# Optimization experiments

Hardware: AMD Instinct MI355X
Metric: run time of the kernel (lower is better)

Reference implementation:

```python
import jax, jax.numpy as jnp
import numpy as np

B, N, H = 8, 1024, 768
NUM_HEADS = 12
HEAD_DIM = H // NUM_HEADS
EDGE_VOCAB = 32
SCALE = 1.0 / np.sqrt(HEAD_DIM)


def setup_inputs() -> dict:
    key = jax.random.key(0)
    ks = jax.random.split(key, 12)
    s = 0.02
    return {
        "x": jax.random.normal(ks[0], (B, N, H), dtype=jnp.float32),
        "E": jax.random.randint(ks[1], (B, N, N), 0, EDGE_VOCAB, dtype=jnp.int64),
        "M": jax.random.randint(ks[2], (B, N), 0, 2, dtype=jnp.int32),
        "Wq": jax.random.normal(ks[3], (H, H), dtype=jnp.float32) * s,
        "bq": jnp.zeros((H,), dtype=jnp.float32),
        "Wk": jax.random.normal(ks[4], (H, H), dtype=jnp.float32) * s,
        "bk": jnp.zeros((H,), dtype=jnp.float32),
        "Wv": jax.random.normal(ks[5], (H, H), dtype=jnp.float32) * s,
        "bv": jnp.zeros((H,), dtype=jnp.float32),
        "Wo": jax.random.normal(ks[6], (H, H), dtype=jnp.float32) * s,
        "bo": jnp.zeros((H,), dtype=jnp.float32),
        "edge_emb": jax.random.normal(ks[7], (EDGE_VOCAB, NUM_HEADS), dtype=jnp.float32) * s,
    }


def reference(x, E, M, Wq, bq, Wk, bk, Wv, bv, Wo, bo, edge_emb):
    b, n, h = x.shape
    nh, hd = NUM_HEADS, HEAD_DIM
    # projections (y = x @ W + b, W stored as (in, out))
    Q = (x @ Wq + bq).reshape(b, n, nh, hd).transpose(0, 2, 1, 3)  # (B,h,N,d)
    K = (x @ Wk + bk).reshape(b, n, nh, hd).transpose(0, 2, 1, 3)
    V = (x @ Wv + bv).reshape(b, n, nh, hd).transpose(0, 2, 1, 3)
    scores = jnp.einsum('bhnd,bhmd->bhnm', Q, K) * SCALE
    # edge bias: (B,N,N) tokens -> (B,N,N,h) -> (B,h,N,N)
    bias = edge_emb[E].transpose(0, 3, 1, 2)
    scores = scores + bias
    # dual masking: mask key positions (M[j]==0) and query positions (M[i]==0)
    valid = (M[:, None, None, :] != 0) & (M[:, None, :, None] != 0)  # (B,1,N,N)
    scores = jnp.where(valid, scores, -1e9)
    attn = jax.nn.softmax(scores, axis=-1)
    out = jnp.einsum('bhnm,bhmd->bhnd', attn, V)
    out = out.transpose(0, 2, 1, 3).reshape(b, n, h)
    return out @ Wo + bo
```

## Files before the change

kernel.cpp:

```cpp
#include <hip/hip_runtime.h>
#include <stdint.h>

#define DEV __device__ __forceinline__

typedef __attribute__((ext_vector_type(8))) short bf16x8;
typedef __attribute__((ext_vector_type(4))) float f32x4;
typedef __attribute__((ext_vector_type(16))) float f32x16;

DEV unsigned short f2bf(float f) {
  union { float f; uint32_t u; } v; v.f = f;
  uint32_t r = v.u + 0x7fffu + ((v.u >> 16) & 1u);
  return (unsigned short)(r >> 16);
}

DEV void lds_load16(void* dst, const void* src) {
  __builtin_amdgcn_global_load_lds(
      (const __attribute__((address_space(1))) unsigned int*)src,
      (__attribute__((address_space(3))) unsigned int*)dst, 16, 0, 0);
}


__global__ void conv_x_k(const float* __restrict__ x, unsigned short* __restrict__ o) {
  const int i = blockIdx.x * 256 + threadIdx.x;
  const float4 v = ((const float4*)x)[i];
  ushort4 u;
  u.x = f2bf(v.x); u.y = f2bf(v.y); u.z = f2bf(v.z); u.w = f2bf(v.w);
  ((ushort4*)o)[i] = u;
}

__global__ void conv_E_k(const int* __restrict__ E, const int* __restrict__ Mm,
                         uint8_t* __restrict__ E8L) {
  const int tid = blockIdx.x * 256 + threadIdx.x;
  const int k4 = tid & 255;
  const int q = (tid >> 8) & 1023;
  const int b = tid >> 18;
  const uint4 e = ((const uint4*)E)[tid];
  const int mq = Mm[b * 1024 + q];
  const int4 mk = *(const int4*)&Mm[b * 1024 + k4 * 4];
  uint32_t r;
  {
    const uint32_t b0 = (mq && mk.x) ? (e.x & 31u) : 32u;
    const uint32_t b1 = (mq && mk.y) ? (e.y & 31u) : 32u;
    const uint32_t b2 = (mq && mk.z) ? (e.z & 31u) : 32u;
    const uint32_t b3 = (mq && mk.w) ? (e.w & 31u) : 32u;
    r = b0 | (b1 << 8) | (b2 << 16) | (b3 << 24);
  }
  const int kt = k4 >> 4;
  const int k4t = k4 & 15;
  const int h = k4t & 1, c = (k4t >> 1) & 3, a = k4t >> 3;
  const int lane = (h << 5) | (q & 31);
  const int qw = q >> 5;
  const int j = a * 4 + c;
  const size_t rec = ((((size_t)b * 32 + qw) * 16 + kt) * 64 + lane) * 32 + j * 4;
  *(uint32_t*)(E8L + rec) = r;
}

__global__ void transp_w_k(const float* __restrict__ Wq, const float* __restrict__ Wk,
                           const float* __restrict__ Wv, const float* __restrict__ Wo,
                           unsigned short* __restrict__ wtqkv, unsigned short* __restrict__ wot) {
  __shared__ float tile[64][65];
  const int z = blockIdx.z;
  const float* W = (z == 0) ? Wq : (z == 1) ? Wk : (z == 2) ? Wv : Wo;
  unsigned short* D = (z < 3) ? wtqkv + (size_t)z * 768 * 768 : wot;
  const int k0 = blockIdx.x * 64;
  const int c0 = blockIdx.y * 64;
  const int t = threadIdx.x;
#pragma unroll
  for (int i = 0; i < 4; ++i) {
    const int idx = i * 256 + t;
    const int r = idx >> 4;
    const int cq = (idx & 15) * 4;
    const float4 v = *(const float4*)&W[(k0 + r) * 768 + c0 + cq];
    tile[r][cq] = v.x; tile[r][cq + 1] = v.y; tile[r][cq + 2] = v.z; tile[r][cq + 3] = v.w;
  }
  __syncthreads();
#pragma unroll
  for (int i = 0; i < 4; ++i) {
    const int idx = i * 256 + t;
    const int c = idx >> 4;
    const int kq = (idx & 15) * 4;
    ushort4 u;
    u.x = f2bf(tile[kq][c]);     u.y = f2bf(tile[kq + 1][c]);
    u.z = f2bf(tile[kq + 2][c]); u.w = f2bf(tile[kq + 3][c]);
    *(ushort4*)&D[(c0 + c) * 768 + k0 + kq] = u;
  }
}

template <int MODE>
__global__ __launch_bounds__(256, 2)
void gemm_bt(const unsigned short* __restrict__ A, const unsigned short* __restrict__ Bt,
             const float* __restrict__ b0, const float* __restrict__ b1, const float* __restrict__ b2,
             unsigned short* __restrict__ Qb, unsigned short* __restrict__ Kb,
             unsigned short* __restrict__ Vt, float* __restrict__ Fo) {
  __shared__ __attribute__((aligned(16))) unsigned short lds[2][8192];
  const int t = threadIdx.x;
  const int lane = t & 63;
  const int wid = t >> 6;
  const int m0 = blockIdx.x * 128;
  const int n0 = blockIdx.y * 128;
  const int wm = (wid >> 1) * 64;
  const int wn = (wid & 1) * 64;
  const int srow = t & 127;
  const int sk8 = (t >> 7) * 8;

  const unsigned short* gA = A + (m0 + srow) * 768 + sk8;
  const unsigned short* gB = Bt + (n0 + srow) * 768 + sk8;

  const f32x4 Z4 = {0.f, 0.f, 0.f, 0.f};
  f32x4 acc[4][4];
#pragma unroll
  for (int m = 0; m < 4; ++m)
#pragma unroll
    for (int n = 0; n < 4; ++n) acc[m][n] = Z4;

  const int a_off = (lane >> 4) * 1024 + (wm + (lane & 15)) * 8;
  const int b_off = 4096 + (lane >> 4) * 1024 + (wn + (lane & 15)) * 8;

  auto stage = [&](int buf, int kt) {
    unsigned short* dA = &lds[buf][0] + wid * 512;
    unsigned short* dB = &lds[buf][4096] + wid * 512;
    const unsigned short* sA = gA + kt * 32;
    const unsigned short* sB = gB + kt * 32;
    lds_load16(dA, sA);
    lds_load16(dA + 2048, sA + 16);
    lds_load16(dB, sB);
    lds_load16(dB + 2048, sB + 16);
  };

  stage(0, 0);
  int cur = 0;
  for (int kt = 0; kt < 24; ++kt) {
    __syncthreads();
    if (kt + 1 < 24) stage(cur ^ 1, kt + 1);
    bf16x8 av[4], bvv[4];
#pragma unroll
    for (int m = 0; m < 4; ++m) av[m] = *(const bf16x8*)&lds[cur][a_off + m * 128];
#pragma unroll
    for (int n = 0; n < 4; ++n) bvv[n] = *(const bf16x8*)&lds[cur][b_off + n * 128];
#pragma unroll
    for (int m = 0; m < 4; ++m)
#pragma unroll
      for (int n = 0; n < 4; ++n)
        acc[m][n] = __builtin_amdgcn_mfma_f32_16x16x32_bf16(av[m], bvv[n], acc[m][n], 0, 0, 0);
    cur ^= 1;
  }

  const int g = lane >> 4;
  const int c15 = lane & 15;
  if (MODE == 1) {
#pragma unroll
    for (int n = 0; n < 4; ++n) {
      const int col = n0 + wn + n * 16 + c15;
      const float bval = b0[col];
#pragma unroll
      for (int m = 0; m < 4; ++m) {
        const int r0 = m0 + wm + m * 16 + g * 4;
#pragma unroll
        for (int r = 0; r < 4; ++r) Fo[(r0 + r) * 768 + col] = acc[m][n][r] + bval;
      }
    }
  } else {
    const int mat = blockIdx.y / 6;
    const float* bsel = (mat == 0) ? b0 : (mat == 1) ? b1 : b2;
    unsigned short* qk = (mat == 0) ? Qb : Kb;
#pragma unroll
    for (int n = 0; n < 4; ++n) {
      const int cw = (blockIdx.y % 6) * 128 + wn + n * 16 + c15;
      const int hh = cw >> 6, dd = cw & 63;
      const float bval = bsel[cw];
#pragma unroll
      for (int m = 0; m < 4; ++m) {
        const int r0 = m0 + wm + m * 16 + g * 4;
        const int bb = r0 >> 10;
        const int nn = r0 & 1023;
        if (mat < 2) {
          unsigned short* dst = qk + ((bb * 12 + hh) * 1024 + nn) * 64 + dd;
#pragma unroll
          for (int r = 0; r < 4; ++r) dst[r * 64] = f2bf(acc[m][n][r] + bval);
        } else {
          ushort4 w;
          w.x = f2bf(acc[m][n][0] + bval);
          w.y = f2bf(acc[m][n][1] + bval);
          w.z = f2bf(acc[m][n][2] + bval);
          w.w = f2bf(acc[m][n][3] + bval);
          *(ushort4*)&Vt[((bb * 12 + hh) * 64 + dd) * 1024 + nn] = w;
        }
      }
    }
  }
}

__global__ __launch_bounds__(256, 3)
void attn_fused(const unsigned short* __restrict__ Qb, const unsigned short* __restrict__ Kb,
                const unsigned short* __restrict__ Vt, const uint8_t* __restrict__ E8L,
                const float* __restrict__ emb, unsigned short* __restrict__ AO) {
  __shared__ __attribute__((aligned(16))) unsigned short Ks[2][4096];
  __shared__ __attribute__((aligned(16))) unsigned short Vs[2][4096];
  __shared__ float ttab[33];
  __shared__ float red[4][32];

  const int t = threadIdx.x;
  const int lane = t & 63;
  const int wid = t >> 6;
  const int l31 = lane & 31;
  const int hl = lane >> 5;

  const int id = blockIdx.x;
  const int sw = (id & 7) * 96 + (id >> 3);
  const int b = sw / 96;
  const int rem = sw - b * 96;
  const int h = rem >> 3;
  const int qb = rem & 7;
  const int bh = b * 12 + h;
  const int qw = qb * 4 + wid;
  const int q0 = qw * 32;

  if (t < 33) ttab[t] = (t < 32) ? emb[t * 12 + h] * 1.44269504f : -1e30f;

  bf16x8 qf[4];
  {
    const unsigned short* qp = Qb + ((size_t)bh * 1024 + q0 + l31) * 64 + hl * 8;
#pragma unroll
    for (int dc = 0; dc < 4; ++dc) qf[dc] = *(const bf16x8*)(qp + dc * 16);
  }

  auto stageKV = [&](int buf, int kt) {
#pragma unroll
    for (int i = 0; i < 2; ++i) {
      const int c = i * 256 + t;
      const int row = c >> 3, c16 = c & 7;
      const int sc = (c16 ^ (row & 7)) * 8;
      lds_load16(&Ks[buf][i * 2048 + wid * 512],
                 Kb + ((size_t)bh * 1024 + kt * 64 + row) * 64 + sc);
      lds_load16(&Vs[buf][i * 2048 + wid * 512],
                 Vt + ((size_t)bh * 64 + row) * 1024 + kt * 64 + sc);
    }
  };

  const uint8_t* ebase = E8L + (((size_t)(b * 32 + qw)) * 16 * 64 + lane) * 32;

  stageKV(0, 0);
  uint4 e0 = *(const uint4*)(ebase);
  uint4 e1 = *(const uint4*)(ebase + 16);

  const f32x16 Z16 = {0.f};
  f32x16 oacc0 = Z16, oacc1 = Z16;
  float m = -3.0e38f, lsum = 0.f;
  int cur = 0;

  for (int kt = 0; kt < 16; ++kt) {
    __syncthreads();
    if (kt + 1 < 16) stageKV(cur ^ 1, kt + 1);
    uint4 en0, en1;
    if (kt + 1 < 16) {
      en0 = *(const uint4*)(ebase + (kt + 1) * 2048);
      en1 = *(const uint4*)(ebase + (kt + 1) * 2048 + 16);
    }

    f32x16 s0 = Z16, s1 = Z16;
#pragma unroll
    for (int dc = 0; dc < 4; ++dc) {
      const int gch = (dc * 2 + hl);
      const bf16x8 a0 = *(const bf16x8*)((const char*)Ks[cur] +
                         l31 * 128 + ((gch ^ (l31 & 7)) << 4));
      const bf16x8 a1 = *(const bf16x8*)((const char*)Ks[cur] +
                         (32 + l31) * 128 + ((gch ^ ((32 + l31) & 7)) << 4));
      s0 = __builtin_amdgcn_mfma_f32_32x32x16_bf16(a0, qf[dc], s0, 0, 0, 0);
      s1 = __builtin_amdgcn_mfma_f32_32x32x16_bf16(a1, qf[dc], s1, 0, 0, 0);
    }

    const uint32_t ed[8] = {e0.x, e0.y, e0.z, e0.w, e1.x, e1.y, e1.z, e1.w};
    float w0[16], w1[16];
#pragma unroll
    for (int r = 0; r < 16; ++r) {
      const uint32_t d0 = ed[r >> 2], d1 = ed[4 + (r >> 2)];
      const int sh = (r & 3) * 8;
      w0[r] = fmaf(s0[r], 0.18033688f, ttab[(d0 >> sh) & 0xffu]);
      w1[r] = fmaf(s1[r], 0.18033688f, ttab[(d1 >> sh) & 0xffu]);
    }

    float rm = fmaxf(w0[0], w1[0]);
#pragma unroll
    for (int r = 1; r < 16; ++r) rm = fmaxf(rm, fmaxf(w0[r], w1[r]));
    rm = fmaxf(rm, __shfl_xor(rm, 32, 64));

    if (__any(rm > m + 11.5415603f)) {
      const float mn = fmaxf(m, rm);
      const float scl = exp2f(m - mn);
      m = mn;
      lsum *= scl;
#pragma unroll
      for (int r = 0; r < 16; ++r) { oacc0[r] *= scl; oacc1[r] *= scl; }
    }

    float rs0 = 0.f, rs1 = 0.f, rs2 = 0.f, rs3 = 0.f;
#pragma unroll
    for (int r = 0; r < 16; ++r) {
      w0[r] = exp2f(w0[r] - m);
      w1[r] = exp2f(w1[r] - m);
    }
#pragma unroll
    for (int r = 0; r < 4; ++r) {
      rs0 += w0[r];  rs1 += w0[4 + r];
      rs2 += w0[8 + r]; rs3 += w0[12 + r];
      rs0 += w1[r];  rs1 += w1[4 + r];
      rs2 += w1[8 + r]; rs3 += w1[12 + r];
    }
    float rs = (rs0 + rs1) + (rs2 + rs3);
    rs += __shfl_xor(rs, 32, 64);
    lsum += rs;

    uint32_t wd0[8], wd1[8];
#pragma unroll
    for (int j = 0; j < 8; ++j) {
      asm("v_cvt_pk_bf16_f32 %0, %1, %2" : "=v"(wd0[j]) : "v"(w0[2 * j]), "v"(w0[2 * j + 1]));
      asm("v_cvt_pk_bf16_f32 %0, %1, %2" : "=v"(wd1[j]) : "v"(w1[2 * j]), "v"(w1[2 * j + 1]));
    }
#pragma unroll
    for (int cc = 0; cc < 2; ++cc) {
      asm volatile("v_permlane32_swap_b32 %0, %1" : "+v"(wd0[4 * cc]), "+v"(wd0[4 * cc + 2]));
      asm volatile("v_permlane32_swap_b32 %0, %1" : "+v"(wd0[4 * cc + 1]), "+v"(wd0[4 * cc + 3]));
      asm volatile("v_permlane32_swap_b32 %0, %1" : "+v"(wd1[4 * cc]), "+v"(wd1[4 * cc + 2]));
      asm volatile("v_permlane32_swap_b32 %0, %1" : "+v"(wd1[4 * cc + 1]), "+v"(wd1[4 * cc + 3]));
    }

#pragma unroll
    for (int kb = 0; kb < 4; ++kb) {
      union { uint32_t u[4]; bf16x8 v; } fu;
      const uint32_t* wds = (kb < 2) ? wd0 : wd1;
      const int cc = kb & 1;
      fu.u[0] = wds[4 * cc];     fu.u[1] = wds[4 * cc + 1];
      fu.u[2] = wds[4 * cc + 2]; fu.u[3] = wds[4 * cc + 3];
      const int gch = kb * 2 + hl;
      const bf16x8 v0 = *(const bf16x8*)((const char*)Vs[cur] +
                         l31 * 128 + ((gch ^ (l31 & 7)) << 4));
      const bf16x8 v1 = *(const bf16x8*)((const char*)Vs[cur] +
                         (32 + l31) * 128 + ((gch ^ ((32 + l31) & 7)) << 4));
      oacc0 = __builtin_amdgcn_mfma_f32_32x32x16_bf16(fu.v, v0, oacc0, 0, 0, 0);
      oacc1 = __builtin_amdgcn_mfma_f32_32x32x16_bf16(fu.v, v1, oacc1, 0, 0, 0);
    }

    e0 = en0; e1 = en1;
    cur ^= 1;
  }

  red[wid][l31] = 1.0f / lsum;
  __syncthreads();
  unsigned short* aob = AO + ((size_t)b * 1024 + q0) * 768 + h * 64;
#pragma unroll
  for (int j = 0; j < 4; ++j) {
    const f32x4 lv = *(const f32x4*)&red[wid][8 * j + 4 * hl];
#pragma unroll
    for (int rr = 0; rr < 4; ++rr) {
      const int rowq = rr + 8 * j + 4 * hl;
      const int reg = 4 * j + rr;
      aob[rowq * 768 + l31]      = f2bf(oacc0[reg] * lv[rr]);
      aob[rowq * 768 + 32 + l31] = f2bf(oacc1[reg] * lv[rr]);
    }
  }
}


extern "C" void kernel_launch(void* const* d_in, const int* in_sizes, int n_in,
                              void* d_out, int out_size, void* d_ws, size_t ws_size,
                              hipStream_t stream) {
  (void)in_sizes; (void)n_in; (void)out_size; (void)ws_size;
  const float* x = (const float*)d_in[0];
  const int* E = (const int*)d_in[1];
  const int* Mm = (const int*)d_in[2];
  const float* Wq = (const float*)d_in[3];
  const float* bq = (const float*)d_in[4];
  const float* Wk = (const float*)d_in[5];
  const float* bk = (const float*)d_in[6];
  const float* Wv = (const float*)d_in[7];
  const float* bv = (const float*)d_in[8];
  const float* Wo = (const float*)d_in[9];
  const float* bo = (const float*)d_in[10];
  const float* emb = (const float*)d_in[11];
  float* out = (float*)d_out;

  char* w = (char*)d_ws;
  unsigned short* x16 = (unsigned short*)w;
  unsigned short* AO = x16;
  w += (size_t)8192 * 768 * 2;
  unsigned short* wtqkv = (unsigned short*)w; w += (size_t)2304 * 768 * 2;
  unsigned short* wot = (unsigned short*)w;   w += (size_t)768 * 768 * 2;
  unsigned short* Qb = (unsigned short*)w;    w += (size_t)8 * 12 * 1024 * 64 * 2;
  unsigned short* Kb = (unsigned short*)w;    w += (size_t)8 * 12 * 1024 * 64 * 2;
  unsigned short* Vt = (unsigned short*)w;    w += (size_t)8 * 12 * 64 * 1024 * 2;
  uint8_t* E8L = (uint8_t*)w;                 w += (size_t)8 * 1024 * 1024;

  conv_x_k<<<6144, 256, 0, stream>>>(x, x16);
  conv_E_k<<<8192, 256, 0, stream>>>(E, Mm, E8L);
  transp_w_k<<<dim3(12, 12, 4), 256, 0, stream>>>(Wq, Wk, Wv, Wo, wtqkv, wot);
  gemm_bt<0><<<dim3(64, 18), 256, 0, stream>>>(x16, wtqkv, bq, bk, bv, Qb, Kb, Vt, nullptr);
  attn_fused<<<768, 256, 0, stream>>>(Qb, Kb, Vt, E8L, emb, AO);
  gemm_bt<1><<<dim3(64, 6), 256, 0, stream>>>(AO, wot, bo, nullptr, nullptr,
                                              nullptr, nullptr, nullptr, out);
}
```

Measured before the change: 174.1 us.

## Deepen GEMM K-tile, remap blocks per XCD, and raise MFMA priority

```diff
diff --git a/kernel.cpp b/kernel.cpp
--- a/kernel.cpp
+++ b/kernel.cpp
@@ -92,19 +92,20 @@
              const float* __restrict__ b0, const float* __restrict__ b1, const float* __restrict__ b2,
              unsigned short* __restrict__ Qb, unsigned short* __restrict__ Kb,
              unsigned short* __restrict__ Vt, float* __restrict__ Fo) {
-  __shared__ __attribute__((aligned(16))) unsigned short lds[2][8192];
+  __shared__ __attribute__((aligned(16))) unsigned short lds[2][16384];
   const int t = threadIdx.x;
   const int lane = t & 63;
   const int wid = t >> 6;
-  const int m0 = blockIdx.x * 128;
-  const int n0 = blockIdx.y * 128;
+
+  const int id = blockIdx.x;
+  const int xcd = id & 7;
+  const int q = id >> 3;
+  const int bx = xcd * 8 + (q & 7);
+  const int by = q >> 3;
+  const int m0 = bx * 128;
+  const int n0 = by * 128;
   const int wm = (wid >> 1) * 64;
   const int wn = (wid & 1) * 64;
-  const int srow = t & 127;
-  const int sk8 = (t >> 7) * 8;
-
-  const unsigned short* gA = A + (m0 + srow) * 768 + sk8;
-  const unsigned short* gB = Bt + (n0 + srow) * 768 + sk8;
 
   const f32x4 Z4 = {0.f, 0.f, 0.f, 0.f};
   f32x4 acc[4][4];
@@ -113,40 +114,50 @@
 #pragma unroll
     for (int n = 0; n < 4; ++n) acc[m][n] = Z4;
 
-  const int a_off = (lane >> 4) * 1024 + (wm + (lane & 15)) * 8;
-  const int b_off = 4096 + (lane >> 4) * 1024 + (wn + (lane & 15)) * 8;
+  const unsigned short* gA0 = A + (size_t)m0 * 768;
+  const unsigned short* gB0 = Bt + (size_t)n0 * 768;
 
   auto stage = [&](int buf, int kt) {
-    unsigned short* dA = &lds[buf][0] + wid * 512;
-    unsigned short* dB = &lds[buf][4096] + wid * 512;
-    const unsigned short* sA = gA + kt * 32;
-    const unsigned short* sB = gB + kt * 32;
-    lds_load16(dA, sA);
-    lds_load16(dA + 2048, sA + 16);
-    lds_load16(dB, sB);
-    lds_load16(dB + 2048, sB + 16);
+#pragma unroll
+    for (int j = 0; j < 4; ++j) {
+      const int u = j * 256 + t;
+      const int kc = u >> 7;
+      const int row = u & 127;
+      const int dst = (j * 256 + wid * 64) * 8;
+      lds_load16(&lds[buf][dst], gA0 + row * 768 + kt * 64 + kc * 8);
+      lds_load16(&lds[buf][8192 + dst], gB0 + row * 768 + kt * 64 + kc * 8);
+    }
   };
 
   stage(0, 0);
   int cur = 0;
-  for (int kt = 0; kt < 24; ++kt) {
-    __syncthreads();
-    if (kt + 1 < 24) stage(cur ^ 1, kt + 1);
-    bf16x8 av[4], bvv[4];
-#pragma unroll
-    for (int m = 0; m < 4; ++m) av[m] = *(const bf16x8*)&lds[cur][a_off + m * 128];
-#pragma unroll
-    for (int n = 0; n < 4; ++n) bvv[n] = *(const bf16x8*)&lds[cur][b_off + n * 128];
-#pragma unroll
-    for (int m = 0; m < 4; ++m)
-#pragma unroll
-      for (int n = 0; n < 4; ++n)
-        acc[m][n] = __builtin_amdgcn_mfma_f32_16x16x32_bf16(av[m], bvv[n], acc[m][n], 0, 0, 0);
-    cur ^= 1;
-  }
-
   const int g = lane >> 4;
   const int c15 = lane & 15;
+
+  for (int kt = 0; kt < 12; ++kt) {
+    __syncthreads();
+    if (kt + 1 < 12) stage(cur ^ 1, kt + 1);
+#pragma unroll
+    for (int kh = 0; kh < 2; ++kh) {
+      const int kc = kh * 4 + g;
+      bf16x8 av[4], bvv[4];
+#pragma unroll
+      for (int m = 0; m < 4; ++m)
+        av[m] = *(const bf16x8*)&lds[cur][kc * 1024 + (wm + m * 16 + c15) * 8];
+#pragma unroll
+      for (int n = 0; n < 4; ++n)
+        bvv[n] = *(const bf16x8*)&lds[cur][8192 + kc * 1024 + (wn + n * 16 + c15) * 8];
+      __builtin_amdgcn_s_setprio(1);
+#pragma unroll
+      for (int m = 0; m < 4; ++m)
+#pragma unroll
+        for (int n = 0; n < 4; ++n)
+          acc[m][n] = __builtin_amdgcn_mfma_f32_16x16x32_bf16(av[m], bvv[n], acc[m][n], 0, 0, 0);
+      __builtin_amdgcn_s_setprio(0);
+    }
+    cur ^= 1;
+  }
+
   if (MODE == 1) {
 #pragma unroll
     for (int n = 0; n < 4; ++n) {
@@ -160,12 +171,12 @@
       }
     }
   } else {
-    const int mat = blockIdx.y / 6;
+    const int mat = by / 6;
     const float* bsel = (mat == 0) ? b0 : (mat == 1) ? b1 : b2;
     unsigned short* qk = (mat == 0) ? Qb : Kb;
 #pragma unroll
     for (int n = 0; n < 4; ++n) {
-      const int cw = (blockIdx.y % 6) * 128 + wn + n * 16 + c15;
+      const int cw = (by % 6) * 128 + wn + n * 16 + c15;
       const int hh = cw >> 6, dd = cw & 63;
       const float bval = bsel[cw];
 #pragma unroll
@@ -258,6 +269,7 @@
     }
 
     f32x16 s0 = Z16, s1 = Z16;
+    __builtin_amdgcn_s_setprio(1);
 #pragma unroll
     for (int dc = 0; dc < 4; ++dc) {
       const int gch = (dc * 2 + hl);
@@ -268,6 +280,7 @@
       s0 = __builtin_amdgcn_mfma_f32_32x32x16_bf16(a0, qf[dc], s0, 0, 0, 0);
       s1 = __builtin_amdgcn_mfma_f32_32x32x16_bf16(a1, qf[dc], s1, 0, 0, 0);
     }
+    __builtin_amdgcn_s_setprio(0);
 
     const uint32_t ed[8] = {e0.x, e0.y, e0.z, e0.w, e1.x, e1.y, e1.z, e1.w};
     float w0[16], w1[16];
@@ -324,6 +337,7 @@
       asm volatile("v_permlane32_swap_b32 %0, %1" : "+v"(wd1[4 * cc + 1]), "+v"(wd1[4 * cc + 3]));
     }
 
+    __builtin_amdgcn_s_setprio(1);
 #pragma unroll
     for (int kb = 0; kb < 4; ++kb) {
       union { uint32_t u[4]; bf16x8 v; } fu;
@@ -339,6 +353,7 @@
       oacc0 = __builtin_amdgcn_mfma_f32_32x32x16_bf16(fu.v, v0, oacc0, 0, 0, 0);
       oacc1 = __builtin_amdgcn_mfma_f32_32x32x16_bf16(fu.v, v1, oacc1, 0, 0, 0);
     }
+    __builtin_amdgcn_s_setprio(0);
 
     e0 = en0; e1 = en1;
     cur ^= 1;
@@ -393,8 +408,8 @@
   conv_x_k<<<6144, 256, 0, stream>>>(x, x16);
   conv_E_k<<<8192, 256, 0, stream>>>(E, Mm, E8L);
   transp_w_k<<<dim3(12, 12, 4), 256, 0, stream>>>(Wq, Wk, Wv, Wo, wtqkv, wot);
-  gemm_bt<0><<<dim3(64, 18), 256, 0, stream>>>(x16, wtqkv, bq, bk, bv, Qb, Kb, Vt, nullptr);
+  gemm_bt<0><<<1152, 256, 0, stream>>>(x16, wtqkv, bq, bk, bv, Qb, Kb, Vt, nullptr);
   attn_fused<<<768, 256, 0, stream>>>(Qb, Kb, Vt, E8L, emb, AO);
-  gemm_bt<1><<<dim3(64, 6), 256, 0, stream>>>(AO, wot, bo, nullptr, nullptr,
-                                              nullptr, nullptr, nullptr, out);
-}
+  gemm_bt<1><<<384, 256, 0, stream>>>(AO, wot, bo, nullptr, nullptr,
+                                      nullptr, nullptr, nullptr, out);
+}
```

Result: slower. 186.4 us (+7.0%).

## Use 256x256 tiled QKV GEMM, raise attention occupancy, add MFMA priority hints

Applied to the files above, without the earlier changes.

```diff
diff --git a/kernel.cpp b/kernel.cpp
--- a/kernel.cpp
+++ b/kernel.cpp
@@ -86,12 +86,114 @@
   }
 }
 
-template <int MODE>
+__global__ __launch_bounds__(512, 1)
+void gemm256_qkv(const unsigned short* __restrict__ A, const unsigned short* __restrict__ Bt,
+                 const float* __restrict__ b0, const float* __restrict__ b1,
+                 const float* __restrict__ b2,
+                 unsigned short* __restrict__ Qb, unsigned short* __restrict__ Kb,
+                 unsigned short* __restrict__ Vt) {
+  __shared__ __attribute__((aligned(16))) unsigned short lds[2][16384];
+  const int t = threadIdx.x;
+  const int lane = t & 63;
+  const int wid = t >> 6;
+  const int wm2 = wid >> 2;
+  const int wn2 = wid & 3;
+  const int g = lane >> 4;
+  const int c15 = lane & 15;
+
+  const int m0 = blockIdx.x * 256;
+  const int n0 = blockIdx.y * 256;
+
+  const f32x4 Z4 = {0.f, 0.f, 0.f, 0.f};
+  f32x4 acc[8][4];
+#pragma unroll
+  for (int m = 0; m < 8; ++m)
+#pragma unroll
+    for (int n = 0; n < 4; ++n) acc[m][n] = Z4;
+
+  const int srow = t & 255;
+  const int skc = t >> 8;
+  const unsigned short* gA = A + (size_t)(m0 + srow) * 768 + skc * 8;
+  const unsigned short* gB = Bt + (size_t)(n0 + srow) * 768 + skc * 8;
+  const int u0e = (skc * 256 + srow) * 8;
+
+  bf16x8 pA0, pA1, pB0, pB1;
+  auto gload = [&](int kt) {
+    const unsigned short* a = gA + kt * 32;
+    const unsigned short* b = gB + kt * 32;
+    pA0 = *(const bf16x8*)a;
+    pA1 = *(const bf16x8*)(a + 16);
+    pB0 = *(const bf16x8*)b;
+    pB1 = *(const bf16x8*)(b + 16);
+  };
+  auto swrite = [&](int buf) {
+    *(bf16x8*)&lds[buf][u0e] = pA0;
+    *(bf16x8*)&lds[buf][u0e + 4096] = pA1;
+    *(bf16x8*)&lds[buf][8192 + u0e] = pB0;
+    *(bf16x8*)&lds[buf][8192 + u0e + 4096] = pB1;
+  };
+
+  gload(0);
+  swrite(0);
+  gload(1);
+  __syncthreads();
+
+  int cur = 0;
+  for (int kt = 0; kt < 24; ++kt) {
+    bf16x8 av[8], bvv[4];
+#pragma unroll
+    for (int m = 0; m < 8; ++m)
+      av[m] = *(const bf16x8*)&lds[cur][g * 2048 + (wm2 * 128 + m * 16 + c15) * 8];
+#pragma unroll
+    for (int n = 0; n < 4; ++n)
+      bvv[n] = *(const bf16x8*)&lds[cur][8192 + g * 2048 + (wn2 * 64 + n * 16 + c15) * 8];
+#pragma unroll
+    for (int m = 0; m < 8; ++m)
+#pragma unroll
+      for (int n = 0; n < 4; ++n)
+        acc[m][n] = __builtin_amdgcn_mfma_f32_16x16x32_bf16(av[m], bvv[n], acc[m][n], 0, 0, 0);
+    if (kt + 1 < 24) {
+      swrite(cur ^ 1);
+      if (kt + 2 < 24) gload(kt + 2);
+    }
+    __syncthreads();
+    cur ^= 1;
+  }
+
+  const int cwb = n0 + wn2 * 64;
+  const int mat = cwb / 768;
+  const int cwm = cwb - mat * 768;
+  const int hh = cwm >> 6;
+  const float* bsel = (mat == 0) ? b0 : (mat == 1) ? b1 : b2;
+  unsigned short* qk = (mat == 0) ? Qb : Kb;
+#pragma unroll
+  for (int n = 0; n < 4; ++n) {
+    const int dd = n * 16 + c15;
+    const float bval = bsel[hh * 64 + dd];
+#pragma unroll
+    for (int m = 0; m < 8; ++m) {
+      const int r0 = m0 + wm2 * 128 + m * 16 + g * 4;
+      const int bb = r0 >> 10;
+      const int nn = r0 & 1023;
+      if (mat < 2) {
+        unsigned short* dst = qk + ((bb * 12 + hh) * 1024 + nn) * 64 + dd;
+#pragma unroll
+        for (int r = 0; r < 4; ++r) dst[r * 64] = f2bf(acc[m][n][r] + bval);
+      } else {
+        ushort4 w;
+        w.x = f2bf(acc[m][n][0] + bval);
+        w.y = f2bf(acc[m][n][1] + bval);
+        w.z = f2bf(acc[m][n][2] + bval);
+        w.w = f2bf(acc[m][n][3] + bval);
+        *(ushort4*)&Vt[((bb * 12 + hh) * 64 + dd) * 1024 + nn] = w;
+      }
+    }
+  }
+}
+
 __global__ __launch_bounds__(256, 2)
-void gemm_bt(const unsigned short* __restrict__ A, const unsigned short* __restrict__ Bt,
-             const float* __restrict__ b0, const float* __restrict__ b1, const float* __restrict__ b2,
-             unsigned short* __restrict__ Qb, unsigned short* __restrict__ Kb,
-             unsigned short* __restrict__ Vt, float* __restrict__ Fo) {
+void gemm_out(const unsigned short* __restrict__ A, const unsigned short* __restrict__ Bt,
+              const float* __restrict__ b0, float* __restrict__ Fo) {
   __shared__ __attribute__((aligned(16))) unsigned short lds[2][8192];
   const int t = threadIdx.x;
   const int lane = t & 63;
@@ -147,50 +249,20 @@
 
   const int g = lane >> 4;
   const int c15 = lane & 15;
-  if (MODE == 1) {
-#pragma unroll
-    for (int n = 0; n < 4; ++n) {
-      const int col = n0 + wn + n * 16 + c15;
-      const float bval = b0[col];
-#pragma unroll
-      for (int m = 0; m < 4; ++m) {
-        const int r0 = m0 + wm + m * 16 + g * 4;
-#pragma unroll
-        for (int r = 0; r < 4; ++r) Fo[(r0 + r) * 768 + col] = acc[m][n][r] + bval;
-      }
-    }
-  } else {
-    const int mat = blockIdx.y / 6;
-    const float* bsel = (mat == 0) ? b0 : (mat == 1) ? b1 : b2;
-    unsigned short* qk = (mat == 0) ? Qb : Kb;
-#pragma unroll
-    for (int n = 0; n < 4; ++n) {
-      const int cw = (blockIdx.y % 6) * 128 + wn + n * 16 + c15;
-      const int hh = cw >> 6, dd = cw & 63;
-      const float bval = bsel[cw];
-#pragma unroll
-      for (int m = 0; m < 4; ++m) {
-        const int r0 = m0 + wm + m * 16 + g * 4;
-        const int bb = r0 >> 10;
-        const int nn = r0 & 1023;
-        if (mat < 2) {
-          unsigned short* dst = qk + ((bb * 12 + hh) * 1024 + nn) * 64 + dd;
-#pragma unroll
-          for (int r = 0; r < 4; ++r) dst[r * 64] = f2bf(acc[m][n][r] + bval);
-        } else {
-          ushort4 w;
-          w.x = f2bf(acc[m][n][0] + bval);
-          w.y = f2bf(acc[m][n][1] + bval);
-          w.z = f2bf(acc[m][n][2] + bval);
-          w.w = f2bf(acc[m][n][3] + bval);
-          *(ushort4*)&Vt[((bb * 12 + hh) * 64 + dd) * 1024 + nn] = w;
-        }
-      }
-    }
-  }
-}
-
-__global__ __launch_bounds__(256, 3)
+#pragma unroll
+  for (int n = 0; n < 4; ++n) {
+    const int col = n0 + wn + n * 16 + c15;
+    const float bval = b0[col];
+#pragma unroll
+    for (int m = 0; m < 4; ++m) {
+      const int r0 = m0 + wm + m * 16 + g * 4;
+#pragma unroll
+      for (int r = 0; r < 4; ++r) Fo[(r0 + r) * 768 + col] = acc[m][n][r] + bval;
+    }
+  }
+}
+
+__global__ __launch_bounds__(256, 4)
 void attn_fused(const unsigned short* __restrict__ Qb, const unsigned short* __restrict__ Kb,
                 const unsigned short* __restrict__ Vt, const uint8_t* __restrict__ E8L,
                 const float* __restrict__ emb, unsigned short* __restrict__ AO) {
@@ -251,13 +323,14 @@
   for (int kt = 0; kt < 16; ++kt) {
     __syncthreads();
     if (kt + 1 < 16) stageKV(cur ^ 1, kt + 1);
-    uint4 en0, en1;
+    uint4 en0 = e0, en1 = e1;
     if (kt + 1 < 16) {
       en0 = *(const uint4*)(ebase + (kt + 1) * 2048);
       en1 = *(const uint4*)(ebase + (kt + 1) * 2048 + 16);
     }
 
     f32x16 s0 = Z16, s1 = Z16;
+    __builtin_amdgcn_s_setprio(1);
 #pragma unroll
     for (int dc = 0; dc < 4; ++dc) {
       const int gch = (dc * 2 + hl);
@@ -268,6 +341,7 @@
       s0 = __builtin_amdgcn_mfma_f32_32x32x16_bf16(a0, qf[dc], s0, 0, 0, 0);
       s1 = __builtin_amdgcn_mfma_f32_32x32x16_bf16(a1, qf[dc], s1, 0, 0, 0);
     }
+    __builtin_amdgcn_s_setprio(0);
 
     const uint32_t ed[8] = {e0.x, e0.y, e0.z, e0.w, e1.x, e1.y, e1.z, e1.w};
     float w0[16], w1[16];
@@ -324,6 +398,7 @@
       asm volatile("v_permlane32_swap_b32 %0, %1" : "+v"(wd1[4 * cc + 1]), "+v"(wd1[4 * cc + 3]));
     }
 
+    __builtin_amdgcn_s_setprio(1);
 #pragma unroll
     for (int kb = 0; kb < 4; ++kb) {
       union { uint32_t u[4]; bf16x8 v; } fu;
@@ -339,6 +414,7 @@
       oacc0 = __builtin_amdgcn_mfma_f32_32x32x16_bf16(fu.v, v0, oacc0, 0, 0, 0);
       oacc1 = __builtin_amdgcn_mfma_f32_32x32x16_bf16(fu.v, v1, oacc1, 0, 0, 0);
     }
+    __builtin_amdgcn_s_setprio(0);
 
     e0 = en0; e1 = en1;
     cur ^= 1;
@@ -393,8 +469,7 @@
   conv_x_k<<<6144, 256, 0, stream>>>(x, x16);
   conv_E_k<<<8192, 256, 0, stream>>>(E, Mm, E8L);
   transp_w_k<<<dim3(12, 12, 4), 256, 0, stream>>>(Wq, Wk, Wv, Wo, wtqkv, wot);
-  gemm_bt<0><<<dim3(64, 18), 256, 0, stream>>>(x16, wtqkv, bq, bk, bv, Qb, Kb, Vt, nullptr);
+  gemm256_qkv<<<dim3(32, 9), 512, 0, stream>>>(x16, wtqkv, bq, bk, bv, Qb, Kb, Vt);
   attn_fused<<<768, 256, 0, stream>>>(Qb, Kb, Vt, E8L, emb, AO);
-  gemm_bt<1><<<dim3(64, 6), 256, 0, stream>>>(AO, wot, bo, nullptr, nullptr,
-                                              nullptr, nullptr, nullptr, out);
-}
+  gemm_out<<<dim3(64, 6), 256, 0, stream>>>(AO, wot, bo, out);
+}
```

Result: slower. 182.5 us (+4.8%).
